# Optimization experiments

Hardware: AMD Instinct MI355X
Metric: run time of the kernel (lower is better)

Reference implementation:

```python
import jax, jax.numpy as jnp
import numpy as np

DIM = 1536
NH = 12
HD = DIM // NH          # 128
C = HD // 2             # 64 complex freq slots per head
DT = C - 2 * (C // 3)   # 22 temporal
DS = C // 3             # 21 per spatial axis
EPS = 1e-6
M_TAB = 64              # rope table length (>= max(f,h,w))


def _rope_tables():
    def tab(d):
        inv = 1.0 / (10000.0 ** (np.arange(d, dtype=np.float64) / d))
        ang = np.outer(np.arange(M_TAB, dtype=np.float64), inv)
        return np.cos(ang), np.sin(ang)
    ct, st = tab(DT)
    ch, sh = tab(DS)
    cw, sw = tab(DS)
    fc = np.concatenate([ct, ch, cw], axis=1).astype(np.float32)  # [M, 64]
    fs = np.concatenate([st, sh, sw], axis=1).astype(np.float32)
    return jnp.asarray(fc), jnp.asarray(fs)


def setup_inputs() -> dict:
    key = jax.random.key(0)
    ks = jax.random.split(key, 6)
    B, F, H, W = 1, 8, 22, 40
    L = F * H * W  # 7040
    s = 0.02
    x = jax.random.normal(ks[0], (B, L, DIM), jnp.float32)
    Wq = jax.random.normal(ks[1], (DIM, DIM), jnp.float32) * s
    Wk = jax.random.normal(ks[2], (DIM, DIM), jnp.float32) * s
    Wv = jax.random.normal(ks[3], (DIM, DIM), jnp.float32) * s
    Wo = jax.random.normal(ks[4], (DIM, DIM), jnp.float32) * s
    bk2 = jax.random.split(ks[5], 4)
    bq = jax.random.normal(bk2[0], (DIM,), jnp.float32) * s
    bk = jax.random.normal(bk2[1], (DIM,), jnp.float32) * s
    bv = jax.random.normal(bk2[2], (DIM,), jnp.float32) * s
    bo = jax.random.normal(bk2[3], (DIM,), jnp.float32) * s
    fc, fs = _rope_tables()
    return dict(x=x, Wq=Wq, bq=bq, Wk=Wk, bk=bk, Wv=Wv, bv=bv, Wo=Wo, bo=bo,
                gq=jnp.ones((DIM,), jnp.float32), gk=jnp.ones((DIM,), jnp.float32),
                freqs_cos=fc, freqs_sin=fs,
                num_frames=F, grid_h=H, grid_w=W,
                chunk_size=2, sink_size=1, max_attention_size=2640)


def _pos_table(tab, f, h, w):
    # tab: [M, 64] -> per-token [f*h*w, 64] via (t,h,w) axis split [22,21,21]
    t = jnp.broadcast_to(tab[:f, :DT][:, None, None, :], (f, h, w, DT))
    hh = jnp.broadcast_to(tab[:h, DT:DT + DS][None, :, None, :], (f, h, w, DS))
    ww = jnp.broadcast_to(tab[:w, DT + DS:][None, None, :, :], (f, h, w, DS))
    return jnp.concatenate([t, hh, ww], axis=-1).reshape(f * h * w, C)


def _forward(x, Wq, bq, Wk, bk, Wv, bv, Wo, bo, gq, gk, freqs_cos, freqs_sin,
             num_frames, grid_h, grid_w, chunk_size, sink_size, max_attention_size):
    B, L, D = x.shape
    lin = lambda t, W, b: jnp.einsum('bld,ed->ble', t, W) + b
    rms = lambda t, g: t * jax.lax.rsqrt(jnp.mean(t * t, axis=-1, keepdims=True) + EPS) * g

    q = rms(lin(x, Wq, bq), gq).reshape(B, L, NH, HD)
    k = rms(lin(x, Wk, bk), gk).reshape(B, L, NH, HD)
    v = lin(x, Wv, bv).reshape(B, L, NH, HD)

    # causal RoPE (start_frame=0)
    cosL = _pos_table(freqs_cos, num_frames, grid_h, grid_w)  # [L, 64]
    sinL = _pos_table(freqs_sin, num_frames, grid_h, grid_w)

    def rope(t):
        a = t.reshape(B, L, NH, C, 2)
        xr, xi = a[..., 0], a[..., 1]
        co = cosL[None, :, None, :]
        si = sinL[None, :, None, :]
        return jnp.stack([xr * co - xi * si, xr * si + xi * co], axis=-1).reshape(B, L, NH, HD)

    q = rope(q)
    k = rope(k)

    # loop attention, diffusion forcing: chunk i attends [0,(i+1)*block) with sink+window
    frame_seqlen = grid_h * grid_w
    block = frame_seqlen * chunk_size
    total_len = num_frames * frame_seqlen
    sink_end = sink_size * frame_seqlen
    num_chunks = -(-total_len // block)
    scale = 1.0 / (HD ** 0.5)

    def attn(qi, ki, vi):
        s = jnp.einsum('bqnd,bknd->bnqk', qi, ki) * scale
        p = jax.nn.softmax(s, axis=-1)
        return jnp.einsum('bnqk,bknd->bqnd', p, vi)

    outs = []
    for i in range(num_chunks):
        q_start = i * block
        q_end = min((i + 1) * block, total_len)
        qi = q[:, q_start:q_end]
        chunk_end = q_end
        if max_attention_size == -1 or sink_end == 0:
            if max_attention_size == -1:
                ki, vi = k[:, :chunk_end], v[:, :chunk_end]
            else:
                ws = max(0, chunk_end - max_attention_size)
                ki, vi = k[:, ws:chunk_end], v[:, ws:chunk_end]
        else:
            window = max_attention_size - sink_end
            ws = max(sink_end, chunk_end - window)
            ki = jnp.concatenate([k[:, :sink_end], k[:, ws:chunk_end]], axis=1)
            vi = jnp.concatenate([v[:, :sink_end], v[:, ws:chunk_end]], axis=1)
        outs.append(attn(qi, ki, vi))

    o = jnp.concatenate(outs, axis=1).reshape(B, L, D)
    return jnp.einsum('bld,ed->ble', o, Wo) + bo


def reference(x, Wq, bq, Wk, bk, Wv, bv, Wo, bo, gq, gk, freqs_cos, freqs_sin,
              num_frames, grid_h, grid_w, chunk_size, sink_size, max_attention_size):
    return _forward(x, Wq, bq, Wk, bk, Wv, bv, Wo, bo, gq, gk, freqs_cos, freqs_sin,
                    num_frames, grid_h, grid_w, chunk_size, sink_size, max_attention_size)
```

## Files before the change

kernel.cpp:

```cpp
#include <hip/hip_runtime.h>
#include <math.h>

typedef __attribute__((ext_vector_type(8))) short short8;
typedef __attribute__((ext_vector_type(4))) float f32x4;
typedef __attribute__((ext_vector_type(16))) float f32x16;
typedef __attribute__((ext_vector_type(4))) float f4;
typedef __attribute__((ext_vector_type(4))) unsigned short us4;
typedef __attribute__((ext_vector_type(2))) unsigned int u32x2;

#define MFMA16(a,b,c) __builtin_amdgcn_mfma_f32_16x16x32_bf16(a,b,c,0,0,0)
#define MFMA32(a,b,c) __builtin_amdgcn_mfma_f32_32x32x16_bf16(a,b,c,0,0,0)

__device__ __forceinline__ unsigned short f2bf(float f) {
  unsigned int u = __float_as_uint(f);
  u = (u + 0x7FFFu + ((u >> 16) & 1u)) >> 16;
  return (unsigned short)u;
}
__device__ __forceinline__ float bf2f(unsigned short b) {
  return __uint_as_float(((unsigned int)b) << 16);
}
__device__ __forceinline__ unsigned int pk2(float a, float b) {
  unsigned int au = __float_as_uint(a) + 0x8000u;
  unsigned int bu = __float_as_uint(b) + 0x8000u;
  return __builtin_amdgcn_perm(bu, au, 0x07060302u);
}

typedef const __attribute__((address_space(1))) unsigned int* gas_t;
typedef __attribute__((address_space(3))) unsigned int* las_t;
__device__ __forceinline__ void gl16(const void* g, void* l) {
  __builtin_amdgcn_global_load_lds((gas_t)g, (las_t)l, 16, 0, 0);
}

__global__ void cvt_f32_bf16(const float* __restrict__ in,
                             unsigned short* __restrict__ out, int n4) {
  int i = blockIdx.x * blockDim.x + threadIdx.x;
  const int stride = gridDim.x * blockDim.x;
  for (; i < n4; i += stride) {
    f4 v = ((const f4*)in)[i];
    us4 o;
    o[0] = f2bf(v[0]); o[1] = f2bf(v[1]); o[2] = f2bf(v[2]); o[3] = f2bf(v[3]);
    ((us4*)out)[i] = o;
  }
}

__global__ void cvt4_f32_bf16(const float* __restrict__ w0, const float* __restrict__ w1,
                              const float* __restrict__ w2, const float* __restrict__ w3,
                              unsigned short* __restrict__ o0, unsigned short* __restrict__ o1,
                              unsigned short* __restrict__ o2, unsigned short* __restrict__ o3,
                              int n4) {
  const float* in = (blockIdx.y == 0) ? w0 : (blockIdx.y == 1) ? w1 : (blockIdx.y == 2) ? w2 : w3;
  unsigned short* out = (blockIdx.y == 0) ? o0 : (blockIdx.y == 1) ? o1 : (blockIdx.y == 2) ? o2 : o3;
  int i = blockIdx.x * blockDim.x + threadIdx.x;
  const int stride = gridDim.x * blockDim.x;
  for (; i < n4; i += stride) {
    f4 v = ((const f4*)in)[i];
    us4 o;
    o[0] = f2bf(v[0]); o[1] = f2bf(v[1]); o[2] = f2bf(v[2]); o[3] = f2bf(v[3]);
    ((us4*)out)[i] = o;
  }
}

__global__ __launch_bounds__(512, 1)
void gemm8(const unsigned short* __restrict__ A,
           const unsigned short* __restrict__ B,
           const float* __restrict__ bias,
           unsigned short* __restrict__ out)
{
  const int bi = blockIdx.x;
  const int wg = (bi & 7) * 63 + (bi >> 3);
  const int m0 = (wg / 18) * 256, n0 = (wg % 18) * 256;

  const int tid = threadIdx.x;
  const int lane = tid & 63, lg = lane >> 4, lr = lane & 15;
  const int wave = tid >> 6, wr = wave >> 2, wc = wave & 3;

  __shared__ __align__(16) unsigned short SMEM[65536];
  auto Abuf = [&](int b) -> unsigned short* { return SMEM + b * 16384; };
  auto Bbuf = [&](int b) -> unsigned short* { return SMEM + 32768 + b * 16384; };

  f32x4 acc[8][4];
#pragma unroll
  for (int m = 0; m < 8; ++m)
#pragma unroll
    for (int n = 0; n < 4; ++n) acc[m][n] = (f32x4){0.f, 0.f, 0.f, 0.f};

  auto stage = [&](const unsigned short* P, int rowBase, int t, unsigned short* lbase) {
    const int k0 = t * 64;
#pragma unroll
    for (int i = 0; i < 2; ++i) {
      int s = i * 512 + tid;
      int row = s >> 3, c = s & 7;
      int cc = c ^ (row & 7);
      gl16(P + (long)(rowBase + row) * 1536 + k0 + cc * 8, (char*)lbase + s * 16);
    }
  };
  auto rdA = [&](int buf, int mr, int k) -> short8 {
    int row = mr + lr;
    int byte = (row * 128 + (k + lg * 8) * 2) ^ ((row & 7) << 4);
    return *(const short8*)((const char*)Abuf(buf) + byte);
  };
  auto rdB = [&](int buf, int nr, int k) -> short8 {
    int row = nr + lr;
    int byte = (row * 128 + (k + lg * 8) * 2) ^ ((row & 7) << 4);
    return *(const short8*)((const char*)Bbuf(buf) + byte);
  };

  stage(A, m0,       0, Abuf(0));
  stage(A, m0 + 128, 0, Abuf(0) + 128 * 64);
  stage(B, n0,       0, Bbuf(0));
  stage(B, n0 + 128, 0, Bbuf(0) + 128 * 64);
  stage(B, n0,       1, Bbuf(1));
  stage(B, n0 + 128, 1, Bbuf(1) + 128 * 64);
  asm volatile("s_waitcnt vmcnt(4)" ::: "memory");
  __builtin_amdgcn_s_barrier();

  for (int T = 0; T < 24; ++T) {
    const int cur = T & 1;
    const int tA = (T + 1 < 24) ? T + 1 : 23;
    const int tB = (T + 2 < 24) ? T + 2 : 23;
    short8 bfr[4][2];
#pragma unroll
    for (int p = 0; p < 4; ++p) {
      if (p == 0)      stage(A, m0,       tA, Abuf(cur ^ 1));
      else if (p == 1) stage(A, m0 + 128, tA, Abuf(cur ^ 1) + 128 * 64);
      else if (p == 2) stage(B, n0,       tB, Bbuf(cur));
      else             stage(B, n0 + 128, tB, Bbuf(cur) + 128 * 64);
      if (p == 0) {
#pragma unroll
        for (int n = 0; n < 4; ++n) {
          bfr[n][0] = rdB(cur, wc * 64 + n * 16, 0);
          bfr[n][1] = rdB(cur, wc * 64 + n * 16, 32);
        }
      }
      short8 afr[2][2];
#pragma unroll
      for (int m2 = 0; m2 < 2; ++m2) {
        afr[m2][0] = rdA(cur, wr * 128 + p * 32 + m2 * 16, 0);
        afr[m2][1] = rdA(cur, wr * 128 + p * 32 + m2 * 16, 32);
      }
      if (p == 3) asm volatile("s_waitcnt vmcnt(4)" ::: "memory");
      __builtin_amdgcn_s_barrier();
      __builtin_amdgcn_s_setprio(1);
#pragma unroll
      for (int m2 = 0; m2 < 2; ++m2)
#pragma unroll
        for (int n = 0; n < 4; ++n) {
          acc[p * 2 + m2][n] = MFMA16(afr[m2][0], bfr[n][0], acc[p * 2 + m2][n]);
          acc[p * 2 + m2][n] = MFMA16(afr[m2][1], bfr[n][1], acc[p * 2 + m2][n]);
        }
      __builtin_amdgcn_s_setprio(0);
      __builtin_amdgcn_s_barrier();
    }
  }
  asm volatile("s_waitcnt vmcnt(0)" ::: "memory");
  __builtin_amdgcn_s_barrier();

#pragma unroll
  for (int n = 0; n < 4; ++n) {
    const int col = wc * 64 + n * 16 + lr;
    const float bs = bias[n0 + col];
#pragma unroll
    for (int m = 0; m < 8; ++m) {
      const int rowb = wr * 128 + m * 16 + lg * 4;
#pragma unroll
      for (int r = 0; r < 4; ++r) {
        int row = rowb + r;
        int byte = row * 512 + ((col * 2) ^ ((row & 7) << 4));
        *(unsigned short*)((char*)SMEM + byte) = f2bf(acc[m][n][r] + bs);
      }
    }
  }
  __builtin_amdgcn_s_barrier();
#pragma unroll
  for (int it = 0; it < 16; ++it) {
    int s = it * 512 + tid;
    int row = s >> 5, c16 = s & 31;
    int byte = row * 512 + ((c16 * 16) ^ ((row & 7) << 4));
    short8 v = *(const short8*)((const char*)SMEM + byte);
    int grow = m0 + row;
    if (grow < 7040)
      *(short8*)(out + (long)grow * 4608 + n0 + c16 * 8) = v;
  }
}

__global__ __launch_bounds__(256)
void gemm_bt(const unsigned short* __restrict__ A,
             const unsigned short* __restrict__ B,
             const float* __restrict__ bias,
             float* __restrict__ of32,
             int K, int ldo, int nbx, int q, int r)
{
  const int lin = blockIdx.x;
  const int xcd = lin & 7, local = lin >> 3;
  const int wg = (xcd < r) ? (xcd * (q + 1) + local) : (r * (q + 1) + (xcd - r) * q + local);
  const int m0 = (wg / nbx) * 128, n0 = (wg % nbx) * 128;

  const int tid = threadIdx.x;
  const int wave = tid >> 6, lane = tid & 63, lg = lane >> 4, lr = lane & 15;
  const int wr = wave >> 1, wc = wave & 1;

  __shared__ __align__(16) unsigned short Al[128 * 32];
  __shared__ __align__(16) unsigned short Bl[128 * 32];

  f32x4 acc[4][4];
#pragma unroll
  for (int m = 0; m < 4; ++m)
#pragma unroll
    for (int n = 0; n < 4; ++n) acc[m][n] = (f32x4){0.f, 0.f, 0.f, 0.f};

  const int r0 = tid >> 2, r1 = (tid + 256) >> 2;
  const int c0 = (tid & 3) * 8;
  const long arow0 = (long)(m0 + r0) * K, arow1 = (long)(m0 + r1) * K;
  const long brow0 = (long)(n0 + r0) * K, brow1 = (long)(n0 + r1) * K;

  for (int k0 = 0; k0 < K; k0 += 32) {
    gl16(A + arow0 + k0 + c0, (char*)Al + tid * 16);
    gl16(A + arow1 + k0 + c0, (char*)Al + (tid + 256) * 16);
    gl16(B + brow0 + k0 + c0, (char*)Bl + tid * 16);
    gl16(B + brow1 + k0 + c0, (char*)Bl + (tid + 256) * 16);
    __syncthreads();
    short8 af[4], bf[4];
#pragma unroll
    for (int m = 0; m < 4; ++m)
      af[m] = *(const short8*)(Al + (wr * 64 + m * 16 + lr) * 32 + lg * 8);
#pragma unroll
    for (int n = 0; n < 4; ++n)
      bf[n] = *(const short8*)(Bl + (wc * 64 + n * 16 + lr) * 32 + lg * 8);
#pragma unroll
    for (int m = 0; m < 4; ++m)
#pragma unroll
      for (int n = 0; n < 4; ++n)
        acc[m][n] = MFMA16(af[m], bf[n], acc[m][n]);
    __syncthreads();
  }

#pragma unroll
  for (int n = 0; n < 4; ++n) {
    const int col = n0 + wc * 64 + n * 16 + lr;
    const float bs = bias[col];
#pragma unroll
    for (int m = 0; m < 4; ++m) {
      const int row = m0 + wr * 64 + m * 16 + lg * 4;
#pragma unroll
      for (int r2 = 0; r2 < 4; ++r2)
        of32[(long)(row + r2) * ldo + col] = acc[m][n][r2] + bs;
    }
  }
}

__global__ __launch_bounds__(256)
void normrope2(unsigned short* __restrict__ qkv, const float* __restrict__ gq,
               const float* __restrict__ gk,
               const float* __restrict__ fc, const float* __restrict__ fs,
               float qsc)
{
  const int l = blockIdx.x, tid = threadIdx.x;
  __shared__ float rowq[1536], rowk[1536];
  __shared__ float sredq[4], sredk[4];
  unsigned short* rpq = qkv + (long)l * 4608;
  unsigned short* rpk = rpq + 1536;

  float ssq = 0.f, ssk = 0.f;
  if (tid < 192) {
    short8 vq = *(const short8*)(rpq + tid * 8);
    short8 vk = *(const short8*)(rpk + tid * 8);
#pragma unroll
    for (int e = 0; e < 8; ++e) {
      float fq = bf2f((unsigned short)vq[e]);
      float fk = bf2f((unsigned short)vk[e]);
      rowq[tid * 8 + e] = fq; ssq += fq * fq;
      rowk[tid * 8 + e] = fk; ssk += fk * fk;
    }
  }
#pragma unroll
  for (int m = 32; m; m >>= 1) {
    ssq += __shfl_xor(ssq, m, 64);
    ssk += __shfl_xor(ssk, m, 64);
  }
  if ((tid & 63) == 0) { sredq[tid >> 6] = ssq; sredk[tid >> 6] = ssk; }
  __syncthreads();
  const float rsq = rsqrtf((sredq[0] + sredq[1] + sredq[2] + sredq[3]) * (1.f / 1536.f) + 1e-6f);
  const float rsk = rsqrtf((sredk[0] + sredk[1] + sredk[2] + sredk[3]) * (1.f / 1536.f) + 1e-6f);

  const int f_ = l / 880, rem = l % 880, h_ = rem / 40, w_ = rem % 40;
#pragma unroll
  for (int j = 0; j < 3; ++j) {
    int p = tid + j * 256;
    int head = p >> 6, c = p & 63;
    int e = head * 128 + 2 * c;
    int tr = (c < 22) ? f_ : ((c < 43) ? h_ : w_);
    float co = fc[tr * 64 + c], si = fs[tr * 64 + c];
    {
      float xr = rowq[e] * rsq * gq[e];
      float xi = rowq[e + 1] * rsq * gq[e + 1];
      float yr = (xr * co - xi * si) * qsc;
      float yi = (xr * si + xi * co) * qsc;
      *(unsigned int*)(rpq + e) = (unsigned int)f2bf(yr) | ((unsigned int)f2bf(yi) << 16);
    }
    {
      float xr = rowk[e] * rsk * gk[e];
      float xi = rowk[e + 1] * rsk * gk[e + 1];
      float yr = xr * co - xi * si;
      float yi = xr * si + xi * co;
      *(unsigned int*)(rpk + e) = (unsigned int)f2bf(yr) | ((unsigned int)f2bf(yi) << 16);
    }
  }
}

__device__ __forceinline__ void issueK(const unsigned short* __restrict__ qkv,
                                       int h, int t, int kvlen, int woff, int tid,
                                       unsigned short* Kbuf)
{
#pragma unroll
  for (int i = 0; i < 4; ++i) {
    int s = i * 256 + tid;
    int kvl = s >> 4;
    int dc = (s & 15) ^ (kvl & 7);
    int j = t * 64 + kvl; j = j < kvlen ? j : kvlen - 1;
    int gk = j + (j >= 880 ? woff : 0);
    gl16(qkv + (long)gk * 4608 + 1536 + h * 128 + dc * 8, (char*)Kbuf + s * 16);
  }
}

__device__ __forceinline__ void loadV(const unsigned short* __restrict__ qkv,
                                      int h, int t, int kvlen, int woff, int tid,
                                      short8 vp[2][2])
{
#pragma unroll
  for (int i = 0; i < 2; ++i) {
    int task = i * 256 + tid;
    int dc = task & 15, kp = task >> 4;
    int kvl = kp * 2;
    int j0 = t * 64 + kvl, j1 = j0 + 1;
    j0 = j0 < kvlen ? j0 : kvlen - 1;
    j1 = j1 < kvlen ? j1 : kvlen - 1;
    int g0 = j0 + (j0 >= 880 ? woff : 0);
    int g1 = j1 + (j1 >= 880 ? woff : 0);
    vp[i][0] = *(const short8*)(qkv + (long)g0 * 4608 + 3072 + h * 128 + dc * 8);
    vp[i][1] = *(const short8*)(qkv + (long)g1 * 4608 + 3072 + h * 128 + dc * 8);
  }
}

__device__ __forceinline__ void writeV(int tid, short8 vp[2][2], unsigned short* Vt)
{
#pragma unroll
  for (int i = 0; i < 2; ++i) {
    int task = i * 256 + tid;
    int dc = task & 15, kp = task >> 4;
    int kvl = kp * 2;
#pragma unroll
    for (int e = 0; e < 8; ++e) {
      int d = dc * 8 + e;
      int byte = d * 128 + kvl * 2;
      byte ^= (((d & 7) ^ ((d >> 3) & 7)) << 4);
      *(unsigned int*)((char*)Vt + byte) =
          (unsigned int)(unsigned short)vp[i][0][e] |
          ((unsigned int)(unsigned short)vp[i][1][e] << 16);
    }
  }
}

__global__ __launch_bounds__(256, 2)
void attn_kern(const unsigned short* __restrict__ qkv,
               unsigned short* __restrict__ ob, int ciBase)
{
  const int qt = blockIdx.x, ci = blockIdx.y + ciBase, h = blockIdx.z;
  const int tid = threadIdx.x, wave = tid >> 6, lane = tid & 63;
  const int l31 = lane & 31, hh = lane >> 5;
  const int chunk_start = ci * 1760, chunk_end = chunk_start + 1760;
  const int wstart = (ci == 0) ? 880 : ci * 1760;
  const int woff = wstart - 880;
  const int kvlen = 880 + (chunk_end - wstart);
  const int q0 = chunk_start + qt * 128;

  __shared__ __align__(16) unsigned short Kl[2][64 * 128];
  __shared__ __align__(16) unsigned short Vt[2][128 * 64];

  int qr = q0 + wave * 32 + l31;
  if (qr >= chunk_end) qr = chunk_end - 1;
  const unsigned short* qp = qkv + (long)qr * 4608 + h * 128;
  short8 qf[8];
#pragma unroll
  for (int st = 0; st < 8; ++st) qf[st] = *(const short8*)(qp + st * 16 + hh * 8);

  f32x16 Oc[4];
#pragma unroll
  for (int i = 0; i < 4; ++i)
#pragma unroll
    for (int j = 0; j < 16; ++j) Oc[i][j] = 0.f;
  float m_run = -1e30f, l_run = 0.f;
  unsigned int w0[8], w1[8];

  auto computeQK = [&](int t, int cur, f32x16* S0, f32x16* S1) {
    f32x16 a0, a1;
#pragma unroll
    for (int j = 0; j < 16; ++j) { a0[j] = 0.f; a1[j] = 0.f; }
    __builtin_amdgcn_s_setprio(1);
#pragma unroll
    for (int st = 0; st < 8; ++st) {
      int off = 32 * st + 16 * hh;
      int b0 = l31 * 256 + (off ^ ((l31 & 7) << 4));
      short8 k0 = *(const short8*)((const char*)&Kl[cur][0] + b0);
      a0 = MFMA32(k0, qf[st], a0);
      int b1 = (32 + l31) * 256 + (off ^ ((l31 & 7) << 4));
      short8 k1 = *(const short8*)((const char*)&Kl[cur][0] + b1);
      a1 = MFMA32(k1, qf[st], a1);
    }
    __builtin_amdgcn_s_setprio(0);
    if (t * 64 + 64 > kvlen) {
#pragma unroll
      for (int r = 0; r < 16; ++r) {
        int kv0 = t * 64 + (r & 3) + 8 * (r >> 2) + 4 * hh;
        if (kv0 >= kvlen)      a0[r] = -1e30f;
        if (kv0 + 32 >= kvlen) a1[r] = -1e30f;
      }
    }
    *S0 = a0; *S1 = a1;
  };

  auto finishTile = [&](f32x16& s0f, f32x16& s1f) {
    float mx[16];
#pragma unroll
    for (int r = 0; r < 16; ++r) mx[r] = fmaxf(s0f[r], s1f[r]);
#pragma unroll
    for (int w = 8; w; w >>= 1)
#pragma unroll
      for (int r = 0; r < w; ++r) mx[r] = fmaxf(mx[r], mx[r + w]);
    float pm = fmaxf(mx[0], __shfl_xor(mx[0], 32, 64));
    const bool defer = __all(pm <= m_run + 8.f);
    const float mn = defer ? m_run : fmaxf(m_run, pm);
#pragma unroll
    for (int r = 0; r < 16; ++r) {
      s0f[r] = __builtin_amdgcn_exp2f(s0f[r] - mn);
      s1f[r] = __builtin_amdgcn_exp2f(s1f[r] - mn);
    }
    float sm[16];
#pragma unroll
    for (int r = 0; r < 16; ++r) sm[r] = s0f[r] + s1f[r];
#pragma unroll
    for (int w = 8; w; w >>= 1)
#pragma unroll
      for (int r = 0; r < w; ++r) sm[r] += sm[r + w];
    float sum = sm[0] + __shfl_xor(sm[0], 32, 64);
    if (defer) {
      l_run += sum;
    } else {
      float al = __builtin_amdgcn_exp2f(m_run - mn);
      l_run = l_run * al + sum;
      m_run = mn;
#pragma unroll
      for (int i = 0; i < 4; ++i)
#pragma unroll
        for (int j = 0; j < 16; ++j) Oc[i][j] *= al;
    }
#pragma unroll
    for (int m = 0; m < 8; ++m) {
      w0[m] = pk2(s0f[2 * m], s0f[2 * m + 1]);
      w1[m] = pk2(s1f[2 * m], s1f[2 * m + 1]);
    }
  };

  auto doPV = [&](int cur) {
    __builtin_amdgcn_s_setprio(1);
#pragma unroll
    for (int s = 0; s < 4; ++s) {
      const unsigned int* w = (s < 2) ? w0 : w1;
      const int lo4 = (s & 1) * 4;
      unsigned int x0 = __shfl_xor(w[lo4 + 2], 32, 64);
      unsigned int x1 = __shfl_xor(w[lo4 + 3], 32, 64);
      unsigned int y0 = __shfl_xor(w[lo4],     32, 64);
      unsigned int y1 = __shfl_xor(w[lo4 + 1], 32, 64);
      unsigned int fw[4];
      fw[0] = hh ? x0 : w[lo4];
      fw[1] = hh ? x1 : w[lo4 + 1];
      fw[2] = hh ? w[lo4 + 2] : y0;
      fw[3] = hh ? w[lo4 + 3] : y1;
      short8 pb = *(const short8*)fw;
#pragma unroll
      for (int dt = 0; dt < 4; ++dt) {
        int d = dt * 32 + l31;
        int byte = d * 128 + s * 32 + hh * 16;
        byte ^= (((d & 7) ^ ((d >> 3) & 7)) << 4);
        short8 vf = *(const short8*)((const char*)&Vt[cur][0] + byte);
        Oc[dt] = MFMA32(vf, pb, Oc[dt]);
      }
    }
    __builtin_amdgcn_s_setprio(0);
  };

  const int nt = (kvlen + 63) >> 6;
  short8 vp[2][2];

  issueK(qkv, h, 0, kvlen, woff, tid, &Kl[0][0]);
  if (nt > 1) issueK(qkv, h, 1, kvlen, woff, tid, &Kl[1][0]);
  loadV(qkv, h, 0, kvlen, woff, tid, vp);
  writeV(tid, vp, &Vt[0][0]);
  __syncthreads();

  f32x16 sp0, sp1;
  computeQK(0, 0, &sp0, &sp1);
  __syncthreads();

  for (int t = 0; t < nt - 1; ++t) {
    const int cur = t & 1;
    if (t + 2 < nt) issueK(qkv, h, t + 2, kvlen, woff, tid, &Kl[cur][0]);
    loadV(qkv, h, t + 1, kvlen, woff, tid, vp);

    f32x16 sc0, sc1;
    computeQK(t + 1, cur ^ 1, &sc0, &sc1);
    finishTile(sp0, sp1);
    writeV(tid, vp, &Vt[cur ^ 1][0]);
    doPV(cur);
    __syncthreads();
    sp0 = sc0; sp1 = sc1;
  }
  finishTile(sp0, sp1);
  doPV((nt - 1) & 1);

  const int qg = q0 + wave * 32 + l31;
  if (qg < chunk_end) {
    const float inv = 1.f / l_run;
    unsigned short* op = ob + (long)qg * 1536 + h * 128;
#pragma unroll
    for (int dt = 0; dt < 4; ++dt) {
#pragma unroll
      for (int gblk = 0; gblk < 4; ++gblk) {
        int d = dt * 32 + gblk * 8 + hh * 4;
        unsigned int u0 = pk2(Oc[dt][4 * gblk]     * inv, Oc[dt][4 * gblk + 1] * inv);
        unsigned int u1 = pk2(Oc[dt][4 * gblk + 2] * inv, Oc[dt][4 * gblk + 3] * inv);
        u32x2 uu; uu[0] = u0; uu[1] = u1;
        *(u32x2*)(op + d) = uu;
      }
    }
  }
}

extern "C" void kernel_launch(void* const* d_in, const int* in_sizes, int n_in,
                              void* d_out, int out_size, void* d_ws, size_t ws_size,
                              hipStream_t stream)
{
  const float* x  = (const float*)d_in[0];
  const float* Wq = (const float*)d_in[1];
  const float* bq = (const float*)d_in[2];
  const float* Wk = (const float*)d_in[3];
  const float* bk = (const float*)d_in[4];
  const float* Wv = (const float*)d_in[5];
  const float* bv = (const float*)d_in[6];
  const float* Wo = (const float*)d_in[7];
  const float* bo = (const float*)d_in[8];
  const float* gq = (const float*)d_in[9];
  const float* gk = (const float*)d_in[10];
  const float* fc = (const float*)d_in[11];
  const float* fs = (const float*)d_in[12];

  char* ws = (char*)d_ws;
  unsigned short* xb   = (unsigned short*)(ws);
  unsigned short* obuf = xb;
  unsigned short* wcat = (unsigned short*)(ws + 22020096);
  unsigned short* wob  = (unsigned short*)(ws + 36175872);
  float*          bcat = (float*)(ws + 40894464);
  unsigned short* qkv  = (unsigned short*)(ws + 40912896);

  cvt_f32_bf16<<<2048, 256, 0, stream>>>(x, xb, 10813440 / 4);
  cvt4_f32_bf16<<<dim3(576, 4), 256, 0, stream>>>(
      Wq, Wk, Wv, Wo,
      wcat, wcat + 2359296, wcat + 4718592, wob, 2359296 / 4);
  hipMemcpyAsync(bcat,        bq, 1536 * 4, hipMemcpyDeviceToDevice, stream);
  hipMemcpyAsync(bcat + 1536, bk, 1536 * 4, hipMemcpyDeviceToDevice, stream);
  hipMemcpyAsync(bcat + 3072, bv, 1536 * 4, hipMemcpyDeviceToDevice, stream);

  gemm8<<<504, 512, 0, stream>>>(xb, wcat, bcat, qkv);

  const float qsc = (float)(1.4426950408889634 / sqrt(128.0));
  normrope2<<<7040, 256, 0, stream>>>(qkv, gq, gk, fc, fs, qsc);

  attn_kern<<<dim3(14, 2, 12), 256, 0, stream>>>(qkv, obuf, 0);
  attn_kern<<<dim3(14, 2, 12), 256, 0, stream>>>(qkv, obuf, 2);

  gemm_bt<<<660, 256, 0, stream>>>(obuf, wob, bo, (float*)d_out, 1536, 1536,
                                   12, 660 / 8, 660 % 8);
}
```

Before: 411.3 us.

## Halve GEMM k-loop phases and merge attention launches into one grid

The QKV GEMM inner loop changes from four sub-phases, each staging one quarter tile with a barrier pair, to two sub-phases. Each phase stages two quarter tiles, reads four A fragments and issues 32 MFMAs. This cuts the barriers per k-step in half but raises register pressure from more live A fragments and makes the loads overlap compute at a coarser grain. Separately, the two attention launches over chunk pairs become a single launch over all four chunks, which removes one launch and its tail gap.

```diff
diff --git a/kernel.cpp b/kernel.cpp
--- a/kernel.cpp
+++ b/kernel.cpp
@@ -119,34 +119,52 @@
     const int tA = (T + 1 < 24) ? T + 1 : 23;
     const int tB = (T + 2 < 24) ? T + 2 : 23;
     short8 bfr[4][2];
-#pragma unroll
-    for (int p = 0; p < 4; ++p) {
-      if (p == 0)      stage(A, m0,       tA, Abuf(cur ^ 1));
-      else if (p == 1) stage(A, m0 + 128, tA, Abuf(cur ^ 1) + 128 * 64);
-      else if (p == 2) stage(B, n0,       tB, Bbuf(cur));
-      else             stage(B, n0 + 128, tB, Bbuf(cur) + 128 * 64);
-      if (p == 0) {
-#pragma unroll
-        for (int n = 0; n < 4; ++n) {
-          bfr[n][0] = rdB(cur, wc * 64 + n * 16, 0);
-          bfr[n][1] = rdB(cur, wc * 64 + n * 16, 32);
-        }
+
+    stage(A, m0,       tA, Abuf(cur ^ 1));
+    stage(A, m0 + 128, tA, Abuf(cur ^ 1) + 128 * 64);
+#pragma unroll
+    for (int n = 0; n < 4; ++n) {
+      bfr[n][0] = rdB(cur, wc * 64 + n * 16, 0);
+      bfr[n][1] = rdB(cur, wc * 64 + n * 16, 32);
+    }
+    {
+      short8 afr[4][2];
+#pragma unroll
+      for (int m2 = 0; m2 < 4; ++m2) {
+        afr[m2][0] = rdA(cur, wr * 128 + m2 * 16, 0);
+        afr[m2][1] = rdA(cur, wr * 128 + m2 * 16, 32);
       }
-      short8 afr[2][2];
-#pragma unroll
-      for (int m2 = 0; m2 < 2; ++m2) {
-        afr[m2][0] = rdA(cur, wr * 128 + p * 32 + m2 * 16, 0);
-        afr[m2][1] = rdA(cur, wr * 128 + p * 32 + m2 * 16, 32);
-      }
-      if (p == 3) asm volatile("s_waitcnt vmcnt(4)" ::: "memory");
       __builtin_amdgcn_s_barrier();
       __builtin_amdgcn_s_setprio(1);
 #pragma unroll
-      for (int m2 = 0; m2 < 2; ++m2)
+      for (int m2 = 0; m2 < 4; ++m2)
 #pragma unroll
         for (int n = 0; n < 4; ++n) {
-          acc[p * 2 + m2][n] = MFMA16(afr[m2][0], bfr[n][0], acc[p * 2 + m2][n]);
-          acc[p * 2 + m2][n] = MFMA16(afr[m2][1], bfr[n][1], acc[p * 2 + m2][n]);
+          acc[m2][n] = MFMA16(afr[m2][0], bfr[n][0], acc[m2][n]);
+          acc[m2][n] = MFMA16(afr[m2][1], bfr[n][1], acc[m2][n]);
+        }
+      __builtin_amdgcn_s_setprio(0);
+      __builtin_amdgcn_s_barrier();
+    }
+
+    stage(B, n0,       tB, Bbuf(cur));
+    stage(B, n0 + 128, tB, Bbuf(cur) + 128 * 64);
+    {
+      short8 afr[4][2];
+#pragma unroll
+      for (int m2 = 0; m2 < 4; ++m2) {
+        afr[m2][0] = rdA(cur, wr * 128 + 64 + m2 * 16, 0);
+        afr[m2][1] = rdA(cur, wr * 128 + 64 + m2 * 16, 32);
+      }
+      asm volatile("s_waitcnt vmcnt(4)" ::: "memory");
+      __builtin_amdgcn_s_barrier();
+      __builtin_amdgcn_s_setprio(1);
+#pragma unroll
+      for (int m2 = 0; m2 < 4; ++m2)
+#pragma unroll
+        for (int n = 0; n < 4; ++n) {
+          acc[4 + m2][n] = MFMA16(afr[m2][0], bfr[n][0], acc[4 + m2][n]);
+          acc[4 + m2][n] = MFMA16(afr[m2][1], bfr[n][1], acc[4 + m2][n]);
         }
       __builtin_amdgcn_s_setprio(0);
       __builtin_amdgcn_s_barrier();
@@ -362,9 +380,9 @@
 
 __global__ __launch_bounds__(256, 2)
 void attn_kern(const unsigned short* __restrict__ qkv,
-               unsigned short* __restrict__ ob, int ciBase)
-{
-  const int qt = blockIdx.x, ci = blockIdx.y + ciBase, h = blockIdx.z;
+               unsigned short* __restrict__ ob)
+{
+  const int qt = blockIdx.x, ci = blockIdx.y, h = blockIdx.z;
   const int tid = threadIdx.x, wave = tid >> 6, lane = tid & 63;
   const int l31 = lane & 31, hh = lane >> 5;
   const int chunk_start = ci * 1760, chunk_end = chunk_start + 1760;
@@ -574,8 +592,7 @@
   const float qsc = (float)(1.4426950408889634 / sqrt(128.0));
   normrope2<<<7040, 256, 0, stream>>>(qkv, gq, gk, fc, fs, qsc);
 
-  attn_kern<<<dim3(14, 2, 12), 256, 0, stream>>>(qkv, obuf, 0);
-  attn_kern<<<dim3(14, 2, 12), 256, 0, stream>>>(qkv, obuf, 2);
+  attn_kern<<<dim3(14, 4, 12), 256, 0, stream>>>(qkv, obuf);
 
   gemm_bt<<<660, 256, 0, stream>>>(obuf, wob, bo, (float*)d_out, 1536, 1536,
                                    12, 660 / 8, 660 % 8);
```

After: 393.9 us, median of 3. -4.2%, faster.
